# Kernel optimization log

Measured on AMD Instinct MI355X. Metric: run time of the kernel, lower is better.

Reference implementation:

```python
import jax, jax.numpy as jnp
import numpy as np

B, T, S, D, H, DK = 2, 2048, 2048, 1024, 16, 64


def setup_inputs() -> dict:
    key = jax.random.key(0)
    ks = jax.random.split(key, 11)
    s = 1.0 / np.sqrt(D)
    return {
        "query": jax.random.normal(ks[0], (B, T, D), jnp.float32),
        "value": jax.random.normal(ks[1], (B, S, D), jnp.float32),
        "key": jax.random.normal(ks[2], (B, S, D), jnp.float32),
        "Wq": jax.random.normal(ks[3], (D, H, DK), jnp.float32) * s,
        "bq": jnp.zeros((H, DK), jnp.float32),
        "Wk": jax.random.normal(ks[4], (D, H, DK), jnp.float32) * s,
        "bk": jnp.zeros((H, DK), jnp.float32),
        "Wv": jax.random.normal(ks[5], (D, H, DK), jnp.float32) * s,
        "bv": jnp.zeros((H, DK), jnp.float32),
        "Wo": jax.random.normal(ks[6], (H, DK, D), jnp.float32) * (1.0 / np.sqrt(H * DK)),
        "bo": jnp.zeros((D,), jnp.float32),
    }


def reference(query, value, key, Wq, bq, Wk, bk, Wv, bv, Wo, bo):
    # Projections: (B, seq, D) x (D, H, DK) -> (B, seq, H, DK)
    q = jnp.einsum("btd,dhk->bthk", query, Wq) + bq
    k = jnp.einsum("bsd,dhk->bshk", key, Wk) + bk
    v = jnp.einsum("bsd,dhk->bshk", value, Wv) + bv
    # Scaled dot-product attention (keras scales query by 1/sqrt(key_dim))
    q = q * (1.0 / np.sqrt(DK)).astype(np.float32)
    scores = jnp.einsum("bshk,bthk->bhts", k, q)  # (B, H, T, S)
    probs = jax.nn.softmax(scores, axis=-1)
    attn = jnp.einsum("bhts,bshk->bthk", probs, v)  # (B, T, H, DK)
    # Output projection back to model dim
    out = jnp.einsum("bthk,hkd->btd", attn, Wo) + bo
    return out
```

## Files before the change

kernel.cpp:

```cpp
#include <hip/hip_runtime.h>
#include <math.h>

#define BB  2
#define TT  2048
#define SSQ 2048
#define DD  1024
#define HH  16
#define DKK 64
#define MM  (BB*TT)
#define NN  (HH*DKK)

typedef __attribute__((ext_vector_type(8))) short short8;
typedef __attribute__((ext_vector_type(4))) float f32x4;
typedef __attribute__((ext_vector_type(2))) unsigned int uint2v;
typedef __attribute__((ext_vector_type(4))) unsigned int u32x4;

__device__ __forceinline__ short f2bf(float x) {
    unsigned u = __builtin_bit_cast(unsigned, x);
    unsigned r = (u + 0x7FFFu + ((u >> 16) & 1u)) >> 16;
    return (short)r;
}

__device__ __forceinline__ unsigned pk2(float lo, float hi) {
    return (__builtin_bit_cast(unsigned, hi) & 0xFFFF0000u) |
           (__builtin_bit_cast(unsigned, lo) >> 16);
}

__device__ __forceinline__ void glds16(const void* g, void* l) {
    __builtin_amdgcn_global_load_lds(
        (const __attribute__((address_space(1))) void*)g,
        (__attribute__((address_space(3))) void*)l, 16, 0, 0);
}

__global__ __launch_bounds__(256)
void to_bf16_acts(const float* __restrict__ a0, const float* __restrict__ a1,
                  const float* __restrict__ a2,
                  short* __restrict__ o0, short* __restrict__ o1,
                  short* __restrict__ o2)
{
    int z = blockIdx.y;
    const float* in = (z == 0) ? a0 : (z == 1) ? a1 : a2;
    short* out = (z == 0) ? o0 : (z == 1) ? o1 : o2;
    size_t i0 = ((size_t)blockIdx.x * 256 + threadIdx.x) * 8;
    f32x4 f0 = *(const f32x4*)(in + i0);
    f32x4 f1 = *(const f32x4*)(in + i0 + 4);
    short8 v;
#pragma unroll
    for (int j = 0; j < 4; j++) v[j] = f2bf(f0[j]);
#pragma unroll
    for (int j = 0; j < 4; j++) v[4 + j] = f2bf(f1[j]);
    *(short8*)(out + i0) = v;
}

__global__ __launch_bounds__(256)
void wtrans(const float* __restrict__ w0, const float* __restrict__ w1,
            const float* __restrict__ w2, const float* __restrict__ w3,
            short* __restrict__ t0, short* __restrict__ t1,
            short* __restrict__ t2, short* __restrict__ t3)
{
    __shared__ float Ls[64][65];
    int z = blockIdx.z;
    const float* in = (z == 0) ? w0 : (z == 1) ? w1 : (z == 2) ? w2 : w3;
    short* out = (z == 0) ? t0 : (z == 1) ? t1 : (z == 2) ? t2 : t3;
    const int r0 = blockIdx.y * 64, c0 = blockIdx.x * 64;
    const int t = threadIdx.x;
    const int r = t >> 2, c4 = t & 3;

    const float* src = in + (size_t)(r0 + r) * DD + c0 + c4 * 16;
#pragma unroll
    for (int i = 0; i < 4; i++) {
        f32x4 f = *(const f32x4*)(src + i * 4);
#pragma unroll
        for (int j = 0; j < 4; j++) Ls[r][c4 * 16 + i * 4 + j] = f[j];
    }
    __syncthreads();

    short8 va, vb;
#pragma unroll
    for (int j = 0; j < 8; j++) va[j] = f2bf(Ls[c4 * 16 + j][r]);
#pragma unroll
    for (int j = 0; j < 8; j++) vb[j] = f2bf(Ls[c4 * 16 + 8 + j][r]);
    short* dst = out + (size_t)(c0 + r) * DD + r0 + c4 * 16;
    *(short8*)dst = va;
    *(short8*)(dst + 8) = vb;
}

__global__ __launch_bounds__(256)
void vtrans(const short* __restrict__ in, short* __restrict__ out)
{
    __shared__ short Ls[64][72];
    const int bh = blockIdx.y;
    const int t0 = blockIdx.x * 64;
    const int tid = threadIdx.x;
    const int r = tid >> 2, c4 = tid & 3;

    const short* src = in + ((size_t)bh * TT + t0 + r) * DKK + c4 * 16;
    *(short8*)&Ls[r][c4 * 16]     = *(const short8*)(src);
    *(short8*)&Ls[r][c4 * 16 + 8] = *(const short8*)(src + 8);
    __syncthreads();

    short8 a, b;
#pragma unroll
    for (int j = 0; j < 8; j++) a[j] = Ls[c4 * 16 + j][r];
#pragma unroll
    for (int j = 0; j < 8; j++) b[j] = Ls[c4 * 16 + 8 + j][r];
    short* dst = out + ((size_t)bh * DKK + r) * SSQ + t0 + c4 * 16;
    *(short8*)dst = a;
    *(short8*)(dst + 8) = b;
}

__device__ __forceinline__ void gemm_core(const short* __restrict__ A,
                                          const short* __restrict__ Bt,
                                          int m0, int n0,
                                          short* As, short* Bs,
                                          f32x4 (&acc)[4][4])
{
    const int tid = threadIdx.x;
    const int w = tid >> 6, l = tid & 63;
    const int l15 = l & 15, quad = l >> 4;
    const int wm = w >> 1, wn = w & 1;

#pragma unroll
    for (int i = 0; i < 4; i++)
#pragma unroll
        for (int j = 0; j < 4; j++) acc[i][j] = (f32x4){0.f, 0.f, 0.f, 0.f};

    const int r = tid >> 2, cseg = tid & 3;
    const short* gA = A + (size_t)(m0 + r) * DD + cseg * 8;
    const short* gB = Bt + (size_t)(n0 + r) * DD + cseg * 8;
    short* ldsA = As + w * 512;
    short* ldsB = Bs + w * 512;

    for (int k0 = 0; k0 < DD; k0 += 32) {
        glds16(gA + k0,                 ldsA);
        glds16(gA + (size_t)64 * DD + k0, ldsA + 2048);
        glds16(gB + k0,                 ldsB);
        glds16(gB + (size_t)64 * DD + k0, ldsB + 2048);
        __syncthreads();

        short8 bF[4];
#pragma unroll
        for (int ni = 0; ni < 4; ni++)
            bF[ni] = *(const short8*)&Bs[(wn * 64 + ni * 16 + l15) * 32 + quad * 8];
#pragma unroll
        for (int mi = 0; mi < 4; mi++) {
            short8 aF = *(const short8*)&As[(wm * 64 + mi * 16 + l15) * 32 + quad * 8];
#pragma unroll
            for (int ni = 0; ni < 4; ni++)
                acc[mi][ni] = __builtin_amdgcn_mfma_f32_16x16x32_bf16(aF, bF[ni], acc[mi][ni], 0, 0, 0);
        }
        __syncthreads();
    }
}

__global__ __launch_bounds__(256, 3)
void gemm_qkv(const short* __restrict__ Aq, const short* __restrict__ Ak,
              const short* __restrict__ Av,
              const short* __restrict__ Wqt, const short* __restrict__ Wkt,
              const short* __restrict__ Wvt,
              const float* __restrict__ bq, const float* __restrict__ bk,
              const float* __restrict__ bv,
              short* __restrict__ Qb, short* __restrict__ Kb,
              short* __restrict__ Vtmp)
{
    __shared__ short As[128 * 32];
    __shared__ short Bs[128 * 32];
    const int z = blockIdx.z;
    const short* A  = (z == 0) ? Aq : (z == 1) ? Ak : Av;
    const short* Bt = (z == 0) ? Wqt : (z == 1) ? Wkt : Wvt;
    const float* bias = (z == 0) ? bq : (z == 1) ? bk : bv;
    short* dst = (z == 0) ? Qb : (z == 1) ? Kb : Vtmp;
    const int m0 = blockIdx.y * 128, n0 = blockIdx.x * 128;

    f32x4 acc[4][4];
    gemm_core(A, Bt, m0, n0, As, Bs, acc);

    const int tid = threadIdx.x;
    const int w = tid >> 6, l = tid & 63;
    const int l15 = l & 15, quad = l >> 4;
    const int wm = w >> 1, wn = w & 1;
    const float scale = (z == 0) ? 0.1803368801f : 1.0f;

#pragma unroll
    for (int mi = 0; mi < 4; mi++) {
#pragma unroll
        for (int reg = 0; reg < 4; reg++) {
            int m = m0 + wm * 64 + mi * 16 + quad * 4 + reg;
            int b = m >> 11, t = m & 2047;
#pragma unroll
            for (int ni = 0; ni < 4; ni++) {
                int n = n0 + wn * 64 + ni * 16 + l15;
                float vv = (acc[mi][ni][reg] + bias[n]) * scale;
                int h = n >> 6, dk = n & 63;
                dst[((size_t)(b * HH + h) * TT + t) * DKK + dk] = f2bf(vv);
            }
        }
    }
}

__global__ __launch_bounds__(256, 3)
void gemm_out(const short* __restrict__ Ab, const short* __restrict__ Wot,
              const float* __restrict__ bo, float* __restrict__ out)
{
    __shared__ short As[64 * 32];
    __shared__ short Bs[128 * 32];
    const int m0 = blockIdx.y * 64, n0 = blockIdx.x * 128;
    const int tid = threadIdx.x;
    const int w = tid >> 6, l = tid & 63;
    const int l15 = l & 15, quad = l >> 4;
    const int wm = w >> 1, wn = w & 1;

    f32x4 acc[2][4];
#pragma unroll
    for (int i = 0; i < 2; i++)
#pragma unroll
        for (int j = 0; j < 4; j++) acc[i][j] = (f32x4){0.f, 0.f, 0.f, 0.f};

    const int r = tid >> 2, cseg = tid & 3;
    const short* gA = Ab + (size_t)(m0 + r) * DD + cseg * 8;
    const short* gB = Wot + (size_t)(n0 + r) * DD + cseg * 8;
    short* ldsA = As + w * 512;
    short* ldsB = Bs + w * 512;

    for (int k0 = 0; k0 < DD; k0 += 32) {
        glds16(gA + k0,                   ldsA);
        glds16(gB + k0,                   ldsB);
        glds16(gB + (size_t)64 * DD + k0, ldsB + 2048);
        __syncthreads();

        short8 bF[4];
#pragma unroll
        for (int ni = 0; ni < 4; ni++)
            bF[ni] = *(const short8*)&Bs[(wn * 64 + ni * 16 + l15) * 32 + quad * 8];
#pragma unroll
        for (int mi = 0; mi < 2; mi++) {
            short8 aF = *(const short8*)&As[(wm * 32 + mi * 16 + l15) * 32 + quad * 8];
#pragma unroll
            for (int ni = 0; ni < 4; ni++)
                acc[mi][ni] = __builtin_amdgcn_mfma_f32_16x16x32_bf16(aF, bF[ni], acc[mi][ni], 0, 0, 0);
        }
        __syncthreads();
    }

#pragma unroll
    for (int mi = 0; mi < 2; mi++) {
#pragma unroll
        for (int reg = 0; reg < 4; reg++) {
            int m = m0 + wm * 32 + mi * 16 + quad * 4 + reg;
#pragma unroll
            for (int ni = 0; ni < 4; ni++) {
                int n = n0 + wn * 64 + ni * 16 + l15;
                out[(size_t)m * DD + n] = acc[mi][ni][reg] + bo[n];
            }
        }
    }
}

__global__ __launch_bounds__(256, 4)
void attn_mfma(const short* __restrict__ Qb, const short* __restrict__ Kb,
               const short* __restrict__ Vbt,
               float* __restrict__ O1, float* __restrict__ O2,
               float* __restrict__ l1, float* __restrict__ l2)
{
    __shared__ short KV[2 * 2 * 64 * 72];

    const int tid = threadIdx.x;
    const int w = tid >> 6, l = tid & 63;
    const int l15 = l & 15, quad = l >> 4;

    const int fid = blockIdx.y * 16 + blockIdx.x;
    const int swz = (fid & 7) * 64 + (fid >> 3);
    const int t0 = (swz & 15) * 128;
    const int bh = swz >> 4;
    const int half = blockIdx.z;
    const size_t hb = (size_t)bh * SSQ * DKK;
    const int r = tid >> 2, c4 = tid & 3;
    const int sbase = half * 1024;

    short8 qf[2][2];
#pragma unroll
    for (int mf = 0; mf < 2; mf++)
#pragma unroll
        for (int kk = 0; kk < 2; kk++)
            qf[mf][kk] = *(const short8*)(Qb + hb +
                (size_t)(t0 + 32 * w + 16 * mf + l15) * DKK + kk * 32 + quad * 8);

    const short* gkb = Kb + hb + (size_t)(sbase + r) * DKK + c4 * 16;
    const short* gvb = Vbt + hb + (size_t)r * SSQ + sbase + c4 * 16;
    short8 kr0 = *(const short8*)(gkb + 0);
    short8 kr1 = *(const short8*)(gkb + 8);
    short8 vr0 = *(const short8*)(gvb + 0);
    short8 vr1 = *(const short8*)(gvb + 8);

    f32x4 o[2][4];
#pragma unroll
    for (int mf = 0; mf < 2; mf++)
#pragma unroll
        for (int j = 0; j < 4; j++) o[mf][j] = (f32x4){0.f, 0.f, 0.f, 0.f};
    f32x4 lacc[2] = {(f32x4){0.f, 0.f, 0.f, 0.f}, (f32x4){0.f, 0.f, 0.f, 0.f}};
    const short8 ones = {(short)0x3F80, (short)0x3F80, (short)0x3F80, (short)0x3F80,
                         (short)0x3F80, (short)0x3F80, (short)0x3F80, (short)0x3F80};

    short* skb = KV + r * 72 + c4 * 16;

    for (int s0 = 0; s0 < 1024; s0 += 64) {
        const int dbo = (s0 & 64) ? 9216 : 0;
        *(short8*)(skb + dbo)          = kr0;
        *(short8*)(skb + dbo + 8)      = kr1;
        *(short8*)(skb + dbo + 4608)   = vr0;
        *(short8*)(skb + dbo + 4616)   = vr1;
        if (s0 + 64 < 1024) {
            const short* gk = gkb + (size_t)(s0 + 64) * DKK;
            const short* gv = gvb + (s0 + 64);
            kr0 = *(const short8*)(gk + 0);
            kr1 = *(const short8*)(gk + 8);
            vr0 = *(const short8*)(gv + 0);
            vr1 = *(const short8*)(gv + 8);
        }
        __syncthreads();
        const short* kb_ = KV + dbo;
        const short* vb_ = kb_ + 4608;

        f32x4 sc[4][2];
#pragma unroll
        for (int np = 0; np < 4; np++)
#pragma unroll
            for (int mf = 0; mf < 2; mf++) sc[np][mf] = (f32x4){0.f, 0.f, 0.f, 0.f};
        __builtin_amdgcn_s_setprio(1);
#pragma unroll
        for (int kk = 0; kk < 2; kk++) {
#pragma unroll
            for (int np = 0; np < 4; np++) {
                short8 aK = *(const short8*)&kb_[(16 * np + l15) * 72 + kk * 32 + quad * 8];
                sc[np][0] = __builtin_amdgcn_mfma_f32_16x16x32_bf16(aK, qf[0][kk], sc[np][0], 0, 0, 0);
                sc[np][1] = __builtin_amdgcn_mfma_f32_16x16x32_bf16(aK, qf[1][kk], sc[np][1], 0, 0, 0);
            }
        }
        __builtin_amdgcn_s_setprio(0);

        short8 pa[2][2];
#pragma unroll
        for (int mf = 0; mf < 2; mf++) {
#pragma unroll
            for (int kk = 0; kk < 2; kk++) {
                u32x4 wd;
#pragma unroll
                for (int b = 0; b < 2; b++) {
                    float p00 = __builtin_amdgcn_exp2f(sc[2 * kk][mf][2 * b]);
                    float p01 = __builtin_amdgcn_exp2f(sc[2 * kk][mf][2 * b + 1]);
                    float p10 = __builtin_amdgcn_exp2f(sc[2 * kk + 1][mf][2 * b]);
                    float p11 = __builtin_amdgcn_exp2f(sc[2 * kk + 1][mf][2 * b + 1]);
                    unsigned Xw = pk2(p00, p01);
                    unsigned Yw = pk2(p10, p11);
                    uint2v s1 = __builtin_amdgcn_permlane32_swap(Xw, Yw, false, false);
                    uint2v s2 = __builtin_amdgcn_permlane16_swap(s1[0], s1[1], false, false);
                    wd[b]     = s2[0];
                    wd[2 + b] = s2[1];
                }
                pa[mf][kk] = __builtin_bit_cast(short8, wd);
            }
        }

        __builtin_amdgcn_s_setprio(1);
#pragma unroll
        for (int kk = 0; kk < 2; kk++) {
            lacc[0] = __builtin_amdgcn_mfma_f32_16x16x32_bf16(pa[0][kk], ones, lacc[0], 0, 0, 0);
            lacc[1] = __builtin_amdgcn_mfma_f32_16x16x32_bf16(pa[1][kk], ones, lacc[1], 0, 0, 0);
#pragma unroll
            for (int np = 0; np < 4; np++) {
                short8 bV = *(const short8*)&vb_[(16 * np + l15) * 72 + kk * 32 + quad * 8];
                o[0][np] = __builtin_amdgcn_mfma_f32_16x16x32_bf16(pa[0][kk], bV, o[0][np], 0, 0, 0);
                o[1][np] = __builtin_amdgcn_mfma_f32_16x16x32_bf16(pa[1][kk], bV, o[1][np], 0, 0, 0);
            }
        }
        __builtin_amdgcn_s_setprio(0);
    }

    float* O = half ? O2 : O1;
    float* L = half ? l2 : l1;
    const size_t rowb = (size_t)bh * TT;
#pragma unroll
    for (int mf = 0; mf < 2; mf++) {
#pragma unroll
        for (int reg = 0; reg < 4; reg++) {
            int t = t0 + 32 * w + 16 * mf + quad * 4 + reg;
            if (l15 == 0) L[rowb + t] = lacc[mf][reg];
            float* orow = O + (rowb + t) * DKK;
#pragma unroll
            for (int np = 0; np < 4; np++)
                orow[16 * np + l15] = o[mf][np][reg];
        }
    }
}

__global__ __launch_bounds__(256)
void combine_norm(const float* __restrict__ O1, const float* __restrict__ O2,
                  const float* __restrict__ l1, const float* __restrict__ l2,
                  short* __restrict__ Ab)
{
    size_t g = (size_t)blockIdx.x * 256 + threadIdx.x;
    size_t i0 = g * 8;
    int bh = (int)(i0 >> 17);
    int t  = (int)((i0 >> 6) & 2047);
    int dk = (int)(i0 & 63);
    float inv = 1.f / (l1[(size_t)bh * TT + t] + l2[(size_t)bh * TT + t]);
    f32x4 a0 = *(const f32x4*)(O1 + i0);
    f32x4 a1 = *(const f32x4*)(O1 + i0 + 4);
    f32x4 b0 = *(const f32x4*)(O2 + i0);
    f32x4 b1 = *(const f32x4*)(O2 + i0 + 4);
    short8 v;
#pragma unroll
    for (int j = 0; j < 4; j++) v[j] = f2bf((a0[j] + b0[j]) * inv);
#pragma unroll
    for (int j = 0; j < 4; j++) v[4 + j] = f2bf((a1[j] + b1[j]) * inv);
    int b = bh >> 4, h = bh & 15;
    *(short8*)(Ab + (((size_t)(b * TT + t) * HH + h) * DKK + dk)) = v;
}

extern "C" void kernel_launch(void* const* d_in, const int* in_sizes, int n_in,
                              void* d_out, int out_size, void* d_ws, size_t ws_size,
                              hipStream_t stream)
{
    const float* query = (const float*)d_in[0];
    const float* value = (const float*)d_in[1];
    const float* key   = (const float*)d_in[2];
    const float* Wq    = (const float*)d_in[3];
    const float* bq    = (const float*)d_in[4];
    const float* Wk    = (const float*)d_in[5];
    const float* bk    = (const float*)d_in[6];
    const float* Wv    = (const float*)d_in[7];
    const float* bv    = (const float*)d_in[8];
    const float* Wo    = (const float*)d_in[9];
    const float* bo    = (const float*)d_in[10];
    float* out = (float*)d_out;

    const size_t actE = (size_t)MM * DD;
    const size_t wE   = (size_t)DD * NN;
    short* p = (short*)d_ws;
    short* Aq   = p; p += actE;
    short* Ak   = p; p += actE;
    short* Av   = p; p += actE;
    short* Wqt  = p; p += wE;
    short* Wkt  = p; p += wE;
    short* Wvt  = p; p += wE;
    short* Wot  = p; p += wE;
    short* Qb   = p; p += actE;
    short* Kb   = p; p += actE;
    short* Vtmp = p; p += actE;
    short* Vbt  = p; p += actE;
    short* Ab   = p; p += actE;
    float* O2f  = (float*)p; p += 2 * actE;
    float* O1f  = (float*)Aq;
    float* l1f  = (float*)Av;
    float* l2f  = l1f + (size_t)BB * HH * TT;

    dim3 blk(256);

    to_bf16_acts<<<dim3((unsigned)(actE / 2048), 3), blk, 0, stream>>>(
        query, key, value, Aq, Ak, Av);

    wtrans<<<dim3(16, 16, 4), blk, 0, stream>>>(Wq, Wk, Wv, Wo, Wqt, Wkt, Wvt, Wot);

    gemm_qkv<<<dim3(NN / 128, MM / 128, 3), blk, 0, stream>>>(
        Aq, Ak, Av, Wqt, Wkt, Wvt, bq, bk, bv, Qb, Kb, Vtmp);

    vtrans<<<dim3(TT / 64, BB * HH), blk, 0, stream>>>(Vtmp, Vbt);

    attn_mfma<<<dim3(TT / 128, BB * HH, 2), blk, 0, stream>>>(
        Qb, Kb, Vbt, O1f, O2f, l1f, l2f);

    combine_norm<<<dim3((unsigned)(actE / 2048)), blk, 0, stream>>>(
        O1f, O2f, l1f, l2f, Ab);

    gemm_out<<<dim3(NN / 128, MM / 64), blk, 0, stream>>>(Ab, Wot, bo, out);
}
```

Before: 228.0 us.

## Fuse fp32-to-bf16 conversion and V transpose into double-buffered QKV GEMM

Removes the separate activation-conversion and V-transpose kernels. The QKV GEMM now loads fp32 activations, converts them in registers with packed bf16 conversion instructions, and writes V directly in transposed layout by swapping the MFMA operands. Both GEMMs get double-buffered LDS with a prefetch of the next K tile, so each iteration needs one barrier instead of two. The trade-off is more LDS, fp32 A loads passing through registers instead of direct-to-LDS copies, and strided 2-byte stores in the V epilogue.

Result: slower. 253.5 us (+11.2%).

```diff
diff --git a/kernel.cpp b/kernel.cpp
--- a/kernel.cpp
+++ b/kernel.cpp
@@ -26,30 +26,21 @@
            (__builtin_bit_cast(unsigned, lo) >> 16);
 }
 
+__device__ __forceinline__ short8 cvt8(f32x4 x, f32x4 y) {
+    unsigned r0, r1, r2, r3;
+    asm("v_cvt_pk_bf16_f32 %0, %1, %2" : "=v"(r0) : "v"(x[0]), "v"(x[1]));
+    asm("v_cvt_pk_bf16_f32 %0, %1, %2" : "=v"(r1) : "v"(x[2]), "v"(x[3]));
+    asm("v_cvt_pk_bf16_f32 %0, %1, %2" : "=v"(r2) : "v"(y[0]), "v"(y[1]));
+    asm("v_cvt_pk_bf16_f32 %0, %1, %2" : "=v"(r3) : "v"(y[2]), "v"(y[3]));
+    u32x4 r;
+    r[0] = r0; r[1] = r1; r[2] = r2; r[3] = r3;
+    return __builtin_bit_cast(short8, r);
+}
+
 __device__ __forceinline__ void glds16(const void* g, void* l) {
     __builtin_amdgcn_global_load_lds(
         (const __attribute__((address_space(1))) void*)g,
         (__attribute__((address_space(3))) void*)l, 16, 0, 0);
-}
-
-__global__ __launch_bounds__(256)
-void to_bf16_acts(const float* __restrict__ a0, const float* __restrict__ a1,
-                  const float* __restrict__ a2,
-                  short* __restrict__ o0, short* __restrict__ o1,
-                  short* __restrict__ o2)
-{
-    int z = blockIdx.y;
-    const float* in = (z == 0) ? a0 : (z == 1) ? a1 : a2;
-    short* out = (z == 0) ? o0 : (z == 1) ? o1 : o2;
-    size_t i0 = ((size_t)blockIdx.x * 256 + threadIdx.x) * 8;
-    f32x4 f0 = *(const f32x4*)(in + i0);
-    f32x4 f1 = *(const f32x4*)(in + i0 + 4);
-    short8 v;
-#pragma unroll
-    for (int j = 0; j < 4; j++) v[j] = f2bf(f0[j]);
-#pragma unroll
-    for (int j = 0; j < 4; j++) v[4 + j] = f2bf(f1[j]);
-    *(short8*)(out + i0) = v;
 }
 
 __global__ __launch_bounds__(256)
@@ -85,114 +76,129 @@
     *(short8*)(dst + 8) = vb;
 }
 
-__global__ __launch_bounds__(256)
-void vtrans(const short* __restrict__ in, short* __restrict__ out)
-{
-    __shared__ short Ls[64][72];
-    const int bh = blockIdx.y;
-    const int t0 = blockIdx.x * 64;
-    const int tid = threadIdx.x;
-    const int r = tid >> 2, c4 = tid & 3;
-
-    const short* src = in + ((size_t)bh * TT + t0 + r) * DKK + c4 * 16;
-    *(short8*)&Ls[r][c4 * 16]     = *(const short8*)(src);
-    *(short8*)&Ls[r][c4 * 16 + 8] = *(const short8*)(src + 8);
-    __syncthreads();
-
-    short8 a, b;
-#pragma unroll
-    for (int j = 0; j < 8; j++) a[j] = Ls[c4 * 16 + j][r];
-#pragma unroll
-    for (int j = 0; j < 8; j++) b[j] = Ls[c4 * 16 + 8 + j][r];
-    short* dst = out + ((size_t)bh * DKK + r) * SSQ + t0 + c4 * 16;
-    *(short8*)dst = a;
-    *(short8*)(dst + 8) = b;
-}
-
-__device__ __forceinline__ void gemm_core(const short* __restrict__ A,
-                                          const short* __restrict__ Bt,
-                                          int m0, int n0,
-                                          short* As, short* Bs,
-                                          f32x4 (&acc)[4][4])
-{
-    const int tid = threadIdx.x;
-    const int w = tid >> 6, l = tid & 63;
-    const int l15 = l & 15, quad = l >> 4;
-    const int wm = w >> 1, wn = w & 1;
-
-#pragma unroll
-    for (int i = 0; i < 4; i++)
-#pragma unroll
-        for (int j = 0; j < 4; j++) acc[i][j] = (f32x4){0.f, 0.f, 0.f, 0.f};
-
-    const int r = tid >> 2, cseg = tid & 3;
-    const short* gA = A + (size_t)(m0 + r) * DD + cseg * 8;
-    const short* gB = Bt + (size_t)(n0 + r) * DD + cseg * 8;
-    short* ldsA = As + w * 512;
-    short* ldsB = Bs + w * 512;
-
-    for (int k0 = 0; k0 < DD; k0 += 32) {
-        glds16(gA + k0,                 ldsA);
-        glds16(gA + (size_t)64 * DD + k0, ldsA + 2048);
-        glds16(gB + k0,                 ldsB);
-        glds16(gB + (size_t)64 * DD + k0, ldsB + 2048);
-        __syncthreads();
-
-        short8 bF[4];
-#pragma unroll
-        for (int ni = 0; ni < 4; ni++)
-            bF[ni] = *(const short8*)&Bs[(wn * 64 + ni * 16 + l15) * 32 + quad * 8];
-#pragma unroll
-        for (int mi = 0; mi < 4; mi++) {
-            short8 aF = *(const short8*)&As[(wm * 64 + mi * 16 + l15) * 32 + quad * 8];
-#pragma unroll
-            for (int ni = 0; ni < 4; ni++)
-                acc[mi][ni] = __builtin_amdgcn_mfma_f32_16x16x32_bf16(aF, bF[ni], acc[mi][ni], 0, 0, 0);
-        }
-        __syncthreads();
-    }
-}
-
 __global__ __launch_bounds__(256, 3)
-void gemm_qkv(const short* __restrict__ Aq, const short* __restrict__ Ak,
-              const short* __restrict__ Av,
+void gemm_qkv(const float* __restrict__ Aqf, const float* __restrict__ Akf,
+              const float* __restrict__ Avf,
               const short* __restrict__ Wqt, const short* __restrict__ Wkt,
               const short* __restrict__ Wvt,
               const float* __restrict__ bq, const float* __restrict__ bk,
               const float* __restrict__ bv,
               short* __restrict__ Qb, short* __restrict__ Kb,
-              short* __restrict__ Vtmp)
-{
-    __shared__ short As[128 * 32];
-    __shared__ short Bs[128 * 32];
+              short* __restrict__ Vbt)
+{
+    __shared__ short As[2][128 * 32];
+    __shared__ short Bs[2][128 * 32];
     const int z = blockIdx.z;
-    const short* A  = (z == 0) ? Aq : (z == 1) ? Ak : Av;
+    const float* A  = (z == 0) ? Aqf : (z == 1) ? Akf : Avf;
     const short* Bt = (z == 0) ? Wqt : (z == 1) ? Wkt : Wvt;
     const float* bias = (z == 0) ? bq : (z == 1) ? bk : bv;
-    short* dst = (z == 0) ? Qb : (z == 1) ? Kb : Vtmp;
     const int m0 = blockIdx.y * 128, n0 = blockIdx.x * 128;
-
-    f32x4 acc[4][4];
-    gemm_core(A, Bt, m0, n0, As, Bs, acc);
 
     const int tid = threadIdx.x;
     const int w = tid >> 6, l = tid & 63;
     const int l15 = l & 15, quad = l >> 4;
     const int wm = w >> 1, wn = w & 1;
-    const float scale = (z == 0) ? 0.1803368801f : 1.0f;
-
-#pragma unroll
-    for (int mi = 0; mi < 4; mi++) {
-#pragma unroll
-        for (int reg = 0; reg < 4; reg++) {
-            int m = m0 + wm * 64 + mi * 16 + quad * 4 + reg;
-            int b = m >> 11, t = m & 2047;
-#pragma unroll
-            for (int ni = 0; ni < 4; ni++) {
-                int n = n0 + wn * 64 + ni * 16 + l15;
-                float vv = (acc[mi][ni][reg] + bias[n]) * scale;
+    const int r = tid >> 2, cseg = tid & 3;
+
+    f32x4 acc[4][4];
+#pragma unroll
+    for (int i = 0; i < 4; i++)
+#pragma unroll
+        for (int j = 0; j < 4; j++) acc[i][j] = (f32x4){0.f, 0.f, 0.f, 0.f};
+
+    const float* gA0 = A + (size_t)(m0 + r) * DD + cseg * 8;
+    const float* gA1 = gA0 + (size_t)64 * DD;
+    const short* gB  = Bt + (size_t)(n0 + r) * DD + cseg * 8;
+    const int aoff0 = r * 32 + cseg * 8;
+    const int aoff1 = (64 + r) * 32 + cseg * 8;
+
+    glds16(gB + 0,                &Bs[0][w * 512]);
+    glds16(gB + (size_t)64 * DD,  &Bs[0][2048 + w * 512]);
+    {
+        f32x4 a00 = *(const f32x4*)(gA0);
+        f32x4 a01 = *(const f32x4*)(gA0 + 4);
+        f32x4 a10 = *(const f32x4*)(gA1);
+        f32x4 a11 = *(const f32x4*)(gA1 + 4);
+        *(short8*)&As[0][aoff0] = cvt8(a00, a01);
+        *(short8*)&As[0][aoff1] = cvt8(a10, a11);
+    }
+
+    for (int k0 = 0; k0 < DD; k0 += 32) {
+        const int cur = (k0 >> 5) & 1;
+        __syncthreads();
+        const bool more = (k0 + 32) < DD;
+        f32x4 a00, a01, a10, a11;
+        if (more) {
+            glds16(gB + k0 + 32,                  &Bs[cur ^ 1][w * 512]);
+            glds16(gB + (size_t)64 * DD + k0 + 32, &Bs[cur ^ 1][2048 + w * 512]);
+            a00 = *(const f32x4*)(gA0 + k0 + 32);
+            a01 = *(const f32x4*)(gA0 + k0 + 36);
+            a10 = *(const f32x4*)(gA1 + k0 + 32);
+            a11 = *(const f32x4*)(gA1 + k0 + 36);
+        }
+
+        short8 bF[4];
+#pragma unroll
+        for (int ni = 0; ni < 4; ni++)
+            bF[ni] = *(const short8*)&Bs[cur][(wn * 64 + ni * 16 + l15) * 32 + quad * 8];
+        if (z != 2) {
+#pragma unroll
+            for (int mi = 0; mi < 4; mi++) {
+                short8 aF = *(const short8*)&As[cur][(wm * 64 + mi * 16 + l15) * 32 + quad * 8];
+#pragma unroll
+                for (int ni = 0; ni < 4; ni++)
+                    acc[mi][ni] = __builtin_amdgcn_mfma_f32_16x16x32_bf16(aF, bF[ni], acc[mi][ni], 0, 0, 0);
+            }
+        } else {
+#pragma unroll
+            for (int mi = 0; mi < 4; mi++) {
+                short8 aF = *(const short8*)&As[cur][(wm * 64 + mi * 16 + l15) * 32 + quad * 8];
+#pragma unroll
+                for (int ni = 0; ni < 4; ni++)
+                    acc[ni][mi] = __builtin_amdgcn_mfma_f32_16x16x32_bf16(bF[ni], aF, acc[ni][mi], 0, 0, 0);
+            }
+        }
+
+        if (more) {
+            *(short8*)&As[cur ^ 1][aoff0] = cvt8(a00, a01);
+            *(short8*)&As[cur ^ 1][aoff1] = cvt8(a10, a11);
+        }
+    }
+
+    if (z != 2) {
+        short* dst = (z == 0) ? Qb : Kb;
+        const float scale = (z == 0) ? 0.1803368801f : 1.0f;
+#pragma unroll
+        for (int mi = 0; mi < 4; mi++) {
+#pragma unroll
+            for (int reg = 0; reg < 4; reg++) {
+                int m = m0 + wm * 64 + mi * 16 + quad * 4 + reg;
+                int b = m >> 11, t = m & 2047;
+#pragma unroll
+                for (int ni = 0; ni < 4; ni++) {
+                    int n = n0 + wn * 64 + ni * 16 + l15;
+                    float vv = (acc[mi][ni][reg] + bias[n]) * scale;
+                    int h = n >> 6, dk = n & 63;
+                    dst[((size_t)(b * HH + h) * TT + t) * DKK + dk] = f2bf(vv);
+                }
+            }
+        }
+    } else {
+        const int b = m0 >> 11;
+        const int tl0 = (m0 & 2047) + wm * 64;
+#pragma unroll
+        for (int ni = 0; ni < 4; ni++) {
+#pragma unroll
+            for (int reg = 0; reg < 4; reg++) {
+                int n = n0 + wn * 64 + ni * 16 + quad * 4 + reg;
                 int h = n >> 6, dk = n & 63;
-                dst[((size_t)(b * HH + h) * TT + t) * DKK + dk] = f2bf(vv);
+                float bb = bias[n];
+                short* vrow = Vbt + ((size_t)(b * HH + h) * DKK + dk) * SSQ;
+#pragma unroll
+                for (int mi = 0; mi < 4; mi++) {
+                    int t = tl0 + mi * 16 + l15;
+                    vrow[t] = f2bf(acc[ni][mi][reg] + bb);
+                }
             }
         }
     }
@@ -202,8 +208,8 @@
 void gemm_out(const short* __restrict__ Ab, const short* __restrict__ Wot,
               const float* __restrict__ bo, float* __restrict__ out)
 {
-    __shared__ short As[64 * 32];
-    __shared__ short Bs[128 * 32];
+    __shared__ short As[2][64 * 32];
+    __shared__ short Bs[2][128 * 32];
     const int m0 = blockIdx.y * 64, n0 = blockIdx.x * 128;
     const int tid = threadIdx.x;
     const int w = tid >> 6, l = tid & 63;
@@ -219,27 +225,31 @@
     const int r = tid >> 2, cseg = tid & 3;
     const short* gA = Ab + (size_t)(m0 + r) * DD + cseg * 8;
     const short* gB = Wot + (size_t)(n0 + r) * DD + cseg * 8;
-    short* ldsA = As + w * 512;
-    short* ldsB = Bs + w * 512;
+
+    glds16(gA + 0,               &As[0][w * 512]);
+    glds16(gB + 0,               &Bs[0][w * 512]);
+    glds16(gB + (size_t)64 * DD, &Bs[0][2048 + w * 512]);
 
     for (int k0 = 0; k0 < DD; k0 += 32) {
-        glds16(gA + k0,                   ldsA);
-        glds16(gB + k0,                   ldsB);
-        glds16(gB + (size_t)64 * DD + k0, ldsB + 2048);
+        const int cur = (k0 >> 5) & 1;
         __syncthreads();
+        if (k0 + 32 < DD) {
+            glds16(gA + k0 + 32,                   &As[cur ^ 1][w * 512]);
+            glds16(gB + k0 + 32,                   &Bs[cur ^ 1][w * 512]);
+            glds16(gB + (size_t)64 * DD + k0 + 32, &Bs[cur ^ 1][2048 + w * 512]);
+        }
 
         short8 bF[4];
 #pragma unroll
         for (int ni = 0; ni < 4; ni++)
-            bF[ni] = *(const short8*)&Bs[(wn * 64 + ni * 16 + l15) * 32 + quad * 8];
+            bF[ni] = *(const short8*)&Bs[cur][(wn * 64 + ni * 16 + l15) * 32 + quad * 8];
 #pragma unroll
         for (int mi = 0; mi < 2; mi++) {
-            short8 aF = *(const short8*)&As[(wm * 32 + mi * 16 + l15) * 32 + quad * 8];
+            short8 aF = *(const short8*)&As[cur][(wm * 32 + mi * 16 + l15) * 32 + quad * 8];
 #pragma unroll
             for (int ni = 0; ni < 4; ni++)
                 acc[mi][ni] = __builtin_amdgcn_mfma_f32_16x16x32_bf16(aF, bF[ni], acc[mi][ni], 0, 0, 0);
         }
-        __syncthreads();
     }
 
 #pragma unroll
@@ -437,34 +447,25 @@
     const size_t actE = (size_t)MM * DD;
     const size_t wE   = (size_t)DD * NN;
     short* p = (short*)d_ws;
-    short* Aq   = p; p += actE;
-    short* Ak   = p; p += actE;
-    short* Av   = p; p += actE;
     short* Wqt  = p; p += wE;
     short* Wkt  = p; p += wE;
     short* Wvt  = p; p += wE;
     short* Wot  = p; p += wE;
     short* Qb   = p; p += actE;
     short* Kb   = p; p += actE;
-    short* Vtmp = p; p += actE;
     short* Vbt  = p; p += actE;
     short* Ab   = p; p += actE;
+    float* O1f  = (float*)p; p += 2 * actE;
     float* O2f  = (float*)p; p += 2 * actE;
-    float* O1f  = (float*)Aq;
-    float* l1f  = (float*)Av;
+    float* l1f  = (float*)p; p += 4 * (size_t)BB * HH * TT;
     float* l2f  = l1f + (size_t)BB * HH * TT;
 
     dim3 blk(256);
 
-    to_bf16_acts<<<dim3((unsigned)(actE / 2048), 3), blk, 0, stream>>>(
-        query, key, value, Aq, Ak, Av);
-
     wtrans<<<dim3(16, 16, 4), blk, 0, stream>>>(Wq, Wk, Wv, Wo, Wqt, Wkt, Wvt, Wot);
 
     gemm_qkv<<<dim3(NN / 128, MM / 128, 3), blk, 0, stream>>>(
-        Aq, Ak, Av, Wqt, Wkt, Wvt, bq, bk, bv, Qb, Kb, Vtmp);
-
-    vtrans<<<dim3(TT / 64, BB * HH), blk, 0, stream>>>(Vtmp, Vbt);
+        query, key, value, Wqt, Wkt, Wvt, bq, bk, bv, Qb, Kb, Vbt);
 
     attn_mfma<<<dim3(TT / 128, BB * HH, 2), blk, 0, stream>>>(
         Qb, Kb, Vbt, O1f, O2f, l1f, l2f);
```
